# Performance work log

Hardware: AMD Instinct MI355X
Metric: run time of the kernel (lower is better)

Reference implementation:

```python
import jax, jax.numpy as jnp
import numpy as np

B, N, D = 4, 2048, 512
H, DH = 8, 64  # heads, dim_head; inner_dim = H*DH = 512
SCALE = DH ** -0.5


def setup_inputs() -> dict:
    key = jax.random.key(0)
    kx, kw = jax.random.split(key)
    x = jax.random.normal(kx, (B, N, D), dtype=jnp.float32)
    # torch Linear weight layout: [out_features=3*H*DH, in_features=D]
    W_qkv = jax.random.normal(kw, (3 * H * DH, D), dtype=jnp.float32) * 0.02
    return {"x": x, "W_qkv": W_qkv}


def reference(x, W_qkv):
    b, n, d = x.shape
    # qkv projection (no bias since qkv_bias=False)
    qkv = x @ W_qkv.T                                  # [b, n, 3*H*DH]
    qkv = qkv.reshape(b, n, 3, H, DH).transpose(2, 0, 3, 1, 4)  # [3, b, H, n, DH]
    q, k, v = qkv[0], qkv[1], qkv[2]
    # shifted query: q_cross[t] = q[t-1] for t>=1, q_cross[0] = q[0]
    q_cross = jnp.concatenate([q[:, :, :1, :], q[:, :, :-1, :]], axis=2)
    scores = jnp.einsum("bhqd,bhkd->bhqk", q_cross * SCALE, k)  # [b, H, n, n]
    attn = jax.nn.softmax(scores, axis=-1)
    out = jnp.einsum("bhqk,bhkd->bhqd", attn, v)       # [b, H, n, DH]
    out = out.transpose(0, 2, 1, 3).reshape(b, n, H * DH)
    # to_out is Dropout(0.0) -> identity in eval / p=0
    return out
```

## Files before the change

### kernel.cpp

```cpp
#include <hip/hip_runtime.h>
#include <hip/hip_bf16.h>
#include <stdint.h>

typedef __bf16 bf16_t;
typedef float floatx4 __attribute__((ext_vector_type(4)));
typedef __bf16 bf16x8 __attribute__((ext_vector_type(8)));
typedef __bf16 bf16x4 __attribute__((ext_vector_type(4)));
typedef unsigned int uintx4 __attribute__((ext_vector_type(4)));

#define QSCALE 0.1803368801111204f

__device__ __forceinline__ void gl2lds16(const bf16_t* g, bf16_t* l) {
    __builtin_amdgcn_global_load_lds(
        (const __attribute__((address_space(1))) unsigned int*)g,
        (__attribute__((address_space(3))) unsigned int*)l,
        16, 0, 0);
}

__device__ __forceinline__ unsigned pk2(float lo, float hi) {
    unsigned short a = __builtin_bit_cast(unsigned short, (bf16_t)lo);
    unsigned short b = __builtin_bit_cast(unsigned short, (bf16_t)hi);
    return (unsigned)a | ((unsigned)b << 16);
}

__global__ __launch_bounds__(256) void convert_kernel(const float* __restrict__ x,
                                                      bf16_t* __restrict__ xb,
                                                      const float* __restrict__ w,
                                                      bf16_t* __restrict__ wb,
                                                      int nx4) {
    int i = blockIdx.x * 256 + threadIdx.x;
    const float* in; bf16_t* out; int j;
    if (i < nx4) { in = x; out = xb; j = i; }
    else         { in = w; out = wb; j = i - nx4; }
    float4 v = ((const float4*)in)[j];
    bf16x4 o;
    o.x = (bf16_t)v.x; o.y = (bf16_t)v.y; o.z = (bf16_t)v.z; o.w = (bf16_t)v.w;
    ((bf16x4*)out)[j] = o;
}

__global__ __launch_bounds__(256, 3) void qkv_gemm(const bf16_t* __restrict__ X,
                                                   const bf16_t* __restrict__ W,
                                                   bf16_t* __restrict__ Q,
                                                   bf16_t* __restrict__ K,
                                                   bf16_t* __restrict__ Vt)
{
    __shared__ bf16_t As[2][128 * 64];
    __shared__ bf16_t Bs[2][64 * 64];

    const int tid  = threadIdx.x;
    const int wave = tid >> 6;
    const int lane = tid & 63;
    const int quad = lane >> 4;
    const int lrow = lane & 15;
    const int t7g  = lrow & 7;
    const int wbase = tid & 192;

    int raw = blockIdx.x;
    int xcd = raw & 7;
    int idx = raw >> 3;
    int bx  = xcd * 8 + idx / 24;
    int by  = idx - (idx / 24) * 24;
    const int bm0 = bx * 128;
    const int bn0 = by * 64;
    const int mw = (wave >> 1) * 64;
    const int nw = (wave & 1) * 32;

    floatx4 acc[4][2];
#pragma unroll
    for (int i = 0; i < 4; i++)
#pragma unroll
        for (int j = 0; j < 2; j++) acc[i][j] = (floatx4)0.0f;

    const bf16_t* xb  = X + (size_t)bm0 * 512;
    const bf16_t* wbp = W + (size_t)bn0 * 512;
    const bf16_t* srcA[4];
    const bf16_t* srcB[2];
#pragma unroll
    for (int r = 0; r < 4; ++r) {
        int c = r * 256 + tid;
        int row = c >> 3, kc = c & 7;
        int skc = kc ^ (row & 7);
        srcA[r] = xb + (size_t)row * 512 + skc * 8;
    }
#pragma unroll
    for (int r = 0; r < 2; ++r) {
        int c = r * 256 + tid;
        int row = c >> 3, kc = c & 7;
        int skc = kc ^ (row & 7);
        srcB[r] = wbp + (size_t)row * 512 + skc * 8;
    }

    auto STAGE = [&](int bufI, int k0) {
#pragma unroll
        for (int r = 0; r < 4; ++r)
            gl2lds16(srcA[r] + k0, As[bufI] + (size_t)(r * 256 + wbase) * 8);
#pragma unroll
        for (int r = 0; r < 2; ++r)
            gl2lds16(srcB[r] + k0, Bs[bufI] + (size_t)(r * 256 + wbase) * 8);
    };

    STAGE(0, 0);

#pragma unroll 1
    for (int kb = 0; kb < 8; ++kb) {
        const int buf = kb & 1;
        __syncthreads();
        if (kb < 7) STAGE(buf ^ 1, (kb + 1) * 64);

        const bf16_t* as = As[buf];
        const bf16_t* bs = Bs[buf];
#pragma unroll
        for (int ks = 0; ks < 2; ++ks) {
            bf16x8 af[4], bfr[2];
#pragma unroll
            for (int mi = 0; mi < 4; mi++)
                af[mi] = *(const bf16x8*)(as + (mw + mi * 16 + lrow) * 64 + (((ks * 4 + quad) ^ t7g) << 3));
#pragma unroll
            for (int ni = 0; ni < 2; ni++)
                bfr[ni] = *(const bf16x8*)(bs + (nw + ni * 16 + lrow) * 64 + (((ks * 4 + quad) ^ t7g) << 3));
            __builtin_amdgcn_s_setprio(1);
#pragma unroll
            for (int mi = 0; mi < 4; mi++)
#pragma unroll
                for (int ni = 0; ni < 2; ni++)
                    acc[mi][ni] = __builtin_amdgcn_mfma_f32_16x16x32_bf16(af[mi], bfr[ni], acc[mi][ni], 0, 0, 0);
            __builtin_amdgcn_s_setprio(0);
        }
    }

#pragma unroll
    for (int mi = 0; mi < 4; mi++) {
        int mbase = bm0 + mw + mi * 16 + quad * 4;
        int b = mbase >> 11, n = mbase & 2047;
#pragma unroll
        for (int ni = 0; ni < 2; ni++) {
            int o = bn0 + nw + ni * 16 + lrow;
            int s  = o >> 9;
            int h  = (o >> 6) & 7;
            int dh = o & 63;
            int bh = b * 8 + h;
            if (s == 2) {
                bf16x4 pv;
#pragma unroll
                for (int r = 0; r < 4; r++) pv[r] = (bf16_t)acc[mi][ni][r];
                *(bf16x4*)(Vt + ((size_t)bh * 64 + dh) * 2048 + n) = pv;
            } else if (s == 0) {
#pragma unroll
                for (int r = 0; r < 4; r++)
                    Q[((size_t)bh * 2048 + n + r) * 64 + dh] = (bf16_t)(acc[mi][ni][r] * QSCALE);
            } else {
#pragma unroll
                for (int r = 0; r < 4; r++)
                    K[((size_t)bh * 2048 + n + r) * 64 + dh] = (bf16_t)acc[mi][ni][r];
            }
        }
    }
}

__device__ __forceinline__ void stage_tile(const bf16_t* __restrict__ kb,
                                           const bf16_t* __restrict__ vb,
                                           int kt, bf16_t* ksbuf, bf16_t* vsbuf,
                                           int wave, int lane) {
#pragma unroll
    for (int part = 0; part < 2; ++part) {
        int ch  = part * 256 + wave * 64 + lane;
        int row = ch >> 3, cc = ch & 7;
        int scc = cc ^ (row & 7);
        bf16_t* ldst = ksbuf + (size_t)(part * 256 + wave * 64) * 8;
        gl2lds16(kb + ((size_t)(kt * 64 + row)) * 64 + scc * 8, ldst);
        bf16_t* ldst2 = vsbuf + (size_t)(part * 256 + wave * 64) * 8;
        gl2lds16(vb + (size_t)row * 2048 + kt * 64 + scc * 8, ldst2);
    }
}

__global__ __launch_bounds__(256, 5) void flash_attn(const bf16_t* __restrict__ Q,
                                                     const bf16_t* __restrict__ K,
                                                     const bf16_t* __restrict__ Vt,
                                                     float* __restrict__ Out)
{
    __shared__ bf16_t Ks[2][64 * 64];
    __shared__ bf16_t Vs[2][64 * 64];

    const int tid  = threadIdx.x;
    const int wave = tid >> 6;
    const int lane = tid & 63;
    const int quad = lane >> 4;
    const int c    = lane & 15;
    const int t7   = c & 7;
    const int qhalf = wave >> 1;
    const int khalf = wave & 1;

    int raw = blockIdx.x + (blockIdx.y << 5);
    int swz = (raw & 7) * 128 + (raw >> 3);
    const int qt = swz & 31;
    const int bh = swz >> 5;
    const int b = bh >> 3, h = bh & 7;

    const int bw    = ((c & 4) << 1) | ((c & 8) >> 1) | (c & 3);
    const int brow7 = bw & 7;

    bf16x8 qf[2][2];
#pragma unroll
    for (int mt = 0; mt < 2; ++mt) {
        int qg  = qt * 64 + qhalf * 32 + mt * 16 + c;
        int src = (qg == 0) ? 0 : qg - 1;
        const bf16_t* qbase = Q + ((size_t)bh * 2048 + src) * 64;
        qf[mt][0] = *(const bf16x8*)(qbase + quad * 8);
        qf[mt][1] = *(const bf16x8*)(qbase + 32 + quad * 8);
    }

    floatx4 o[2][4];
#pragma unroll
    for (int mt = 0; mt < 2; ++mt)
#pragma unroll
        for (int i = 0; i < 4; i++) o[mt][i] = (floatx4)0.0f;
    float lacc[2] = {0.f, 0.f};

    const bf16_t* kb = K + ((size_t)bh * 2048) * 64;
    const bf16_t* vb = Vt + ((size_t)bh * 64) * 2048;

    stage_tile(kb, vb, 0, Ks[0], Vs[0], wave, lane);

#pragma unroll 1
    for (int kt = 0; kt < 32; ++kt) {
        const int buf = kt & 1;
        __syncthreads();
        if (kt < 31)
            stage_tile(kb, vb, kt + 1, Ks[buf ^ 1], Vs[buf ^ 1], wave, lane);

        const bf16_t* ks = Ks[buf];
        const bf16_t* vs = Vs[buf];

        floatx4 s[2][2];
        __builtin_amdgcn_s_setprio(1);
#pragma unroll
        for (int nt = 0; nt < 2; ++nt) {
            const bf16_t* krow = ks + (khalf * 32 + nt * 16 + bw) * 64;
            bf16x8 kf0 = *(const bf16x8*)(krow + ((quad ^ brow7) << 3));
            bf16x8 kf1 = *(const bf16x8*)(krow + (((4 + quad) ^ brow7) << 3));
#pragma unroll
            for (int mt = 0; mt < 2; ++mt) {
                floatx4 t = (floatx4)0.0f;
                t = __builtin_amdgcn_mfma_f32_16x16x32_bf16(kf0, qf[mt][0], t, 0, 0, 0);
                t = __builtin_amdgcn_mfma_f32_16x16x32_bf16(kf1, qf[mt][1], t, 0, 0, 0);
                s[mt][nt] = t;
            }
        }
        __builtin_amdgcn_s_setprio(0);

        bf16x8 pfrag[2];
#pragma unroll
        for (int mt = 0; mt < 2; ++mt) {
            float pe[2][4];
#pragma unroll
            for (int nt = 0; nt < 2; ++nt)
#pragma unroll
                for (int r = 0; r < 4; ++r) {
                    float p = __builtin_amdgcn_exp2f(s[mt][nt][r]);
                    lacc[mt] += p;
                    pe[nt][r] = p;
                }
            unsigned A0 = pk2(pe[0][0], pe[0][1]);
            unsigned A1 = pk2(pe[0][2], pe[0][3]);
            unsigned B0 = pk2(pe[1][0], pe[1][1]);
            unsigned B1 = pk2(pe[1][2], pe[1][3]);
            auto r0 = __builtin_amdgcn_permlane32_swap((int)A0, (int)B0, false, false);
            auto r1 = __builtin_amdgcn_permlane32_swap((int)A1, (int)B1, false, false);
            uintx4 fd;
            fd.x = (unsigned)r0[0];
            fd.y = (unsigned)r1[0];
            fd.z = (unsigned)r0[1];
            fd.w = (unsigned)r1[1];
            pfrag[mt] = __builtin_bit_cast(bf16x8, fd);
        }

        __builtin_amdgcn_s_setprio(1);
#pragma unroll
        for (int sub = 0; sub < 4; ++sub) {
            const bf16_t* vrow = vs + (sub * 16 + c) * 64;
            bf16x8 vf = *(const bf16x8*)(vrow + (((khalf * 4 + quad) ^ t7) << 3));
            o[0][sub] = __builtin_amdgcn_mfma_f32_16x16x32_bf16(pfrag[0], vf, o[0][sub], 0, 0, 0);
            o[1][sub] = __builtin_amdgcn_mfma_f32_16x16x32_bf16(pfrag[1], vf, o[1][sub], 0, 0, 0);
        }
        __builtin_amdgcn_s_setprio(0);
    }

#pragma unroll
    for (int mt = 0; mt < 2; ++mt) {
        lacc[mt] += __shfl_xor(lacc[mt], 16, 64);
        lacc[mt] += __shfl_xor(lacc[mt], 32, 64);
    }

    __syncthreads();
    float* obuf = (float*)Ks;
    float* lbuf = (float*)Vs;
    if (khalf == 1) {
#pragma unroll
        for (int mt = 0; mt < 2; ++mt)
#pragma unroll
            for (int sub = 0; sub < 4; ++sub)
                *(floatx4*)(obuf + qhalf * 2048 + (mt * 4 + sub) * 256 + lane * 4) = o[mt][sub];
        if (lane < 16) {
#pragma unroll
            for (int mt = 0; mt < 2; ++mt)
                lbuf[qhalf * 32 + mt * 16 + c] = lacc[mt];
        }
    }
    __syncthreads();
    if (khalf == 0) {
#pragma unroll
        for (int mt = 0; mt < 2; ++mt)
#pragma unroll
            for (int sub = 0; sub < 4; ++sub)
                o[mt][sub] += *(const floatx4*)(obuf + qhalf * 2048 + (mt * 4 + sub) * 256 + lane * 4);
#pragma unroll
        for (int mt = 0; mt < 2; ++mt)
            lacc[mt] += lbuf[qhalf * 32 + mt * 16 + c];

        float* ob = Out + (size_t)b * 2048 * 512 + (size_t)h * 64;
#pragma unroll
        for (int mt = 0; mt < 2; ++mt) {
            int n0 = qt * 64 + qhalf * 32 + mt * 16 + quad * 4;
#pragma unroll
            for (int r = 0; r < 4; r++) {
                float lr = __shfl(lacc[mt], quad * 4 + r, 64);
                float inv = 1.0f / lr;
                float* orow = ob + (size_t)(n0 + r) * 512;
#pragma unroll
                for (int sub = 0; sub < 4; ++sub)
                    orow[sub * 16 + c] = o[mt][sub][r] * inv;
            }
        }
    }
}

extern "C" void kernel_launch(void* const* d_in, const int* in_sizes, int n_in,
                              void* d_out, int out_size, void* d_ws, size_t ws_size,
                              hipStream_t stream) {
    const float* x = (const float*)d_in[0];
    const float* w = (const float*)d_in[1];
    float* out = (float*)d_out;

    char* ws = (char*)d_ws;
    bf16_t* xb = (bf16_t*)(ws);
    bf16_t* wb = (bf16_t*)(ws + 8388608);
    bf16_t* q  = (bf16_t*)(ws + 9961472);
    bf16_t* k  = (bf16_t*)(ws + 18350080);
    bf16_t* vt = (bf16_t*)(ws + 26738688);

    convert_kernel<<<4864, 256, 0, stream>>>(x, xb, w, wb, 1048576);
    qkv_gemm<<<1536, 256, 0, stream>>>(xb, wb, q, k, vt);
    flash_attn<<<dim3(32, 32), 256, 0, stream>>>(q, k, vt, out);
}
```

Measured before the change: 140.9 us.

## Load K and V fragments directly from global memory, dropping LDS staging

Removes the double-buffered LDS staging of K and V tiles and the per-iteration block barrier. Each wave now loads its MFMA fragments straight from global memory into registers and relies on L2/L1 for reuse across the waves that share a head. The occupancy hint drops from 5 to 4 blocks. This saves LDS traffic and synchronisation, but global load latency is now exposed inside the loop with no software prefetch, and each K/V row is fetched by multiple waves.

```diff
diff --git a/kernel.cpp b/kernel.cpp
--- a/kernel.cpp
+++ b/kernel.cpp
@@ -157,36 +157,18 @@
     }
 }
 
-__device__ __forceinline__ void stage_tile(const bf16_t* __restrict__ kb,
-                                           const bf16_t* __restrict__ vb,
-                                           int kt, bf16_t* ksbuf, bf16_t* vsbuf,
-                                           int wave, int lane) {
-#pragma unroll
-    for (int part = 0; part < 2; ++part) {
-        int ch  = part * 256 + wave * 64 + lane;
-        int row = ch >> 3, cc = ch & 7;
-        int scc = cc ^ (row & 7);
-        bf16_t* ldst = ksbuf + (size_t)(part * 256 + wave * 64) * 8;
-        gl2lds16(kb + ((size_t)(kt * 64 + row)) * 64 + scc * 8, ldst);
-        bf16_t* ldst2 = vsbuf + (size_t)(part * 256 + wave * 64) * 8;
-        gl2lds16(vb + (size_t)row * 2048 + kt * 64 + scc * 8, ldst2);
-    }
-}
-
-__global__ __launch_bounds__(256, 5) void flash_attn(const bf16_t* __restrict__ Q,
+__global__ __launch_bounds__(256, 4) void flash_attn(const bf16_t* __restrict__ Q,
                                                      const bf16_t* __restrict__ K,
                                                      const bf16_t* __restrict__ Vt,
                                                      float* __restrict__ Out)
 {
-    __shared__ bf16_t Ks[2][64 * 64];
-    __shared__ bf16_t Vs[2][64 * 64];
+    __shared__ float red[2 * 2048 + 64];
 
     const int tid  = threadIdx.x;
     const int wave = tid >> 6;
     const int lane = tid & 63;
     const int quad = lane >> 4;
     const int c    = lane & 15;
-    const int t7   = c & 7;
     const int qhalf = wave >> 1;
     const int khalf = wave & 1;
 
@@ -196,8 +178,7 @@
     const int bh = swz >> 5;
     const int b = bh >> 3, h = bh & 7;
 
-    const int bw    = ((c & 4) << 1) | ((c & 8) >> 1) | (c & 3);
-    const int brow7 = bw & 7;
+    const int bw = ((c & 4) << 1) | ((c & 8) >> 1) | (c & 3);
 
     bf16x8 qf[2][2];
 #pragma unroll
@@ -216,37 +197,36 @@
         for (int i = 0; i < 4; i++) o[mt][i] = (floatx4)0.0f;
     float lacc[2] = {0.f, 0.f};
 
-    const bf16_t* kb = K + ((size_t)bh * 2048) * 64;
-    const bf16_t* vb = Vt + ((size_t)bh * 64) * 2048;
-
-    stage_tile(kb, vb, 0, Ks[0], Vs[0], wave, lane);
+    const bf16_t* kk = K + ((size_t)bh * 2048 + khalf * 32 + bw) * 64 + quad * 8;
+    const bf16_t* vv = Vt + ((size_t)bh * 64 + c) * 2048 + khalf * 32 + quad * 8;
 
 #pragma unroll 1
     for (int kt = 0; kt < 32; ++kt) {
-        const int buf = kt & 1;
-        __syncthreads();
-        if (kt < 31)
-            stage_tile(kb, vb, kt + 1, Ks[buf ^ 1], Vs[buf ^ 1], wave, lane);
-
-        const bf16_t* ks = Ks[buf];
-        const bf16_t* vs = Vs[buf];
+        bf16x8 kf00 = *(const bf16x8*)(kk);
+        bf16x8 kf01 = *(const bf16x8*)(kk + 32);
+        bf16x8 kf10 = *(const bf16x8*)(kk + 1024);
+        bf16x8 kf11 = *(const bf16x8*)(kk + 1056);
 
         floatx4 s[2][2];
         __builtin_amdgcn_s_setprio(1);
 #pragma unroll
-        for (int nt = 0; nt < 2; ++nt) {
-            const bf16_t* krow = ks + (khalf * 32 + nt * 16 + bw) * 64;
-            bf16x8 kf0 = *(const bf16x8*)(krow + ((quad ^ brow7) << 3));
-            bf16x8 kf1 = *(const bf16x8*)(krow + (((4 + quad) ^ brow7) << 3));
-#pragma unroll
-            for (int mt = 0; mt < 2; ++mt) {
-                floatx4 t = (floatx4)0.0f;
-                t = __builtin_amdgcn_mfma_f32_16x16x32_bf16(kf0, qf[mt][0], t, 0, 0, 0);
-                t = __builtin_amdgcn_mfma_f32_16x16x32_bf16(kf1, qf[mt][1], t, 0, 0, 0);
-                s[mt][nt] = t;
-            }
+        for (int mt = 0; mt < 2; ++mt) {
+            floatx4 t0 = (floatx4)0.0f;
+            t0 = __builtin_amdgcn_mfma_f32_16x16x32_bf16(kf00, qf[mt][0], t0, 0, 0, 0);
+            t0 = __builtin_amdgcn_mfma_f32_16x16x32_bf16(kf01, qf[mt][1], t0, 0, 0, 0);
+            s[mt][0] = t0;
+            floatx4 t1 = (floatx4)0.0f;
+            t1 = __builtin_amdgcn_mfma_f32_16x16x32_bf16(kf10, qf[mt][0], t1, 0, 0, 0);
+            t1 = __builtin_amdgcn_mfma_f32_16x16x32_bf16(kf11, qf[mt][1], t1, 0, 0, 0);
+            s[mt][1] = t1;
         }
         __builtin_amdgcn_s_setprio(0);
+
+        bf16x8 vf0 = *(const bf16x8*)(vv);
+        bf16x8 vf1 = *(const bf16x8*)(vv + 16 * 2048);
+        bf16x8 vf2 = *(const bf16x8*)(vv + 32 * 2048);
+        bf16x8 vf3 = *(const bf16x8*)(vv + 48 * 2048);
+        kk += 4096; vv += 64;
 
         bf16x8 pfrag[2];
 #pragma unroll
@@ -275,13 +255,14 @@
         }
 
         __builtin_amdgcn_s_setprio(1);
-#pragma unroll
-        for (int sub = 0; sub < 4; ++sub) {
-            const bf16_t* vrow = vs + (sub * 16 + c) * 64;
-            bf16x8 vf = *(const bf16x8*)(vrow + (((khalf * 4 + quad) ^ t7) << 3));
-            o[0][sub] = __builtin_amdgcn_mfma_f32_16x16x32_bf16(pfrag[0], vf, o[0][sub], 0, 0, 0);
-            o[1][sub] = __builtin_amdgcn_mfma_f32_16x16x32_bf16(pfrag[1], vf, o[1][sub], 0, 0, 0);
-        }
+        o[0][0] = __builtin_amdgcn_mfma_f32_16x16x32_bf16(pfrag[0], vf0, o[0][0], 0, 0, 0);
+        o[1][0] = __builtin_amdgcn_mfma_f32_16x16x32_bf16(pfrag[1], vf0, o[1][0], 0, 0, 0);
+        o[0][1] = __builtin_amdgcn_mfma_f32_16x16x32_bf16(pfrag[0], vf1, o[0][1], 0, 0, 0);
+        o[1][1] = __builtin_amdgcn_mfma_f32_16x16x32_bf16(pfrag[1], vf1, o[1][1], 0, 0, 0);
+        o[0][2] = __builtin_amdgcn_mfma_f32_16x16x32_bf16(pfrag[0], vf2, o[0][2], 0, 0, 0);
+        o[1][2] = __builtin_amdgcn_mfma_f32_16x16x32_bf16(pfrag[1], vf2, o[1][2], 0, 0, 0);
+        o[0][3] = __builtin_amdgcn_mfma_f32_16x16x32_bf16(pfrag[0], vf3, o[0][3], 0, 0, 0);
+        o[1][3] = __builtin_amdgcn_mfma_f32_16x16x32_bf16(pfrag[1], vf3, o[1][3], 0, 0, 0);
         __builtin_amdgcn_s_setprio(0);
     }
 
@@ -291,9 +272,8 @@
         lacc[mt] += __shfl_xor(lacc[mt], 32, 64);
     }
 
-    __syncthreads();
-    float* obuf = (float*)Ks;
-    float* lbuf = (float*)Vs;
+    float* obuf = red;
+    float* lbuf = red + 4096;
     if (khalf == 1) {
 #pragma unroll
         for (int mt = 0; mt < 2; ++mt)
```

Result: slower. 209.0 us (+48.4%).

## Split keys across all four waves with 128-key stages and tree reduction

Applied to the files above, without the earlier changes.

Each wave now handles all 64 queries of the block against its own 16-key slice of each 64-key tile, instead of a 2x2 split over queries and keys. Two K/V tiles (128 keys) are loaded per iteration without double buffering, with a barrier before and after each load. A two-level LDS reduction then merges the four partial outputs. This halves the loop trip count and increases reuse of each loaded K/V fragment. In exchange the load latency is exposed, register pressure rises (launch bounds drop from 5 to 3), the epilogue reduction is longer, and the block-index swizzle is removed.

```diff
diff --git a/kernel.cpp b/kernel.cpp
--- a/kernel.cpp
+++ b/kernel.cpp
@@ -157,113 +157,112 @@
     }
 }
 
-__device__ __forceinline__ void stage_tile(const bf16_t* __restrict__ kb,
-                                           const bf16_t* __restrict__ vb,
-                                           int kt, bf16_t* ksbuf, bf16_t* vsbuf,
-                                           int wave, int lane) {
-#pragma unroll
-    for (int part = 0; part < 2; ++part) {
-        int ch  = part * 256 + wave * 64 + lane;
-        int row = ch >> 3, cc = ch & 7;
-        int scc = cc ^ (row & 7);
-        bf16_t* ldst = ksbuf + (size_t)(part * 256 + wave * 64) * 8;
-        gl2lds16(kb + ((size_t)(kt * 64 + row)) * 64 + scc * 8, ldst);
-        bf16_t* ldst2 = vsbuf + (size_t)(part * 256 + wave * 64) * 8;
-        gl2lds16(vb + (size_t)row * 2048 + kt * 64 + scc * 8, ldst2);
-    }
-}
-
-__global__ __launch_bounds__(256, 5) void flash_attn(const bf16_t* __restrict__ Q,
+__global__ __launch_bounds__(256, 3) void flash_attn(const bf16_t* __restrict__ Q,
                                                      const bf16_t* __restrict__ K,
                                                      const bf16_t* __restrict__ Vt,
                                                      float* __restrict__ Out)
 {
-    __shared__ bf16_t Ks[2][64 * 64];
-    __shared__ bf16_t Vs[2][64 * 64];
+    __shared__ __align__(16) bf16_t smem[4 * 4096];
+    __shared__ float lbuf[4 * 64];
+
+    bf16_t* Ks = smem;
+    bf16_t* Vs = smem + 8192;
 
     const int tid  = threadIdx.x;
-    const int wave = tid >> 6;
+    const int w    = tid >> 6;
     const int lane = tid & 63;
     const int quad = lane >> 4;
     const int c    = lane & 15;
-    const int t7   = c & 7;
-    const int qhalf = wave >> 1;
-    const int khalf = wave & 1;
-
-    int raw = blockIdx.x + (blockIdx.y << 5);
-    int swz = (raw & 7) * 128 + (raw >> 3);
-    const int qt = swz & 31;
-    const int bh = swz >> 5;
-    const int b = bh >> 3, h = bh & 7;
-
-    const int bw    = ((c & 4) << 1) | ((c & 8) >> 1) | (c & 3);
-    const int brow7 = bw & 7;
-
-    bf16x8 qf[2][2];
-#pragma unroll
-    for (int mt = 0; mt < 2; ++mt) {
-        int qg  = qt * 64 + qhalf * 32 + mt * 16 + c;
+    const int qt = blockIdx.x;
+    const int bh = blockIdx.y;
+    const int b = bh >> 3, hd = bh & 7;
+
+    const int bw  = ((c & 4) << 1) | ((c & 8) >> 1) | (c & 3);
+    const int bw7 = bw & 7;
+
+    bf16x8 qf[4][2];
+#pragma unroll
+    for (int g = 0; g < 4; ++g) {
+        int qg  = qt * 64 + g * 16 + c;
         int src = (qg == 0) ? 0 : qg - 1;
         const bf16_t* qbase = Q + ((size_t)bh * 2048 + src) * 64;
-        qf[mt][0] = *(const bf16x8*)(qbase + quad * 8);
-        qf[mt][1] = *(const bf16x8*)(qbase + 32 + quad * 8);
-    }
-
-    floatx4 o[2][4];
-#pragma unroll
-    for (int mt = 0; mt < 2; ++mt)
-#pragma unroll
-        for (int i = 0; i < 4; i++) o[mt][i] = (floatx4)0.0f;
-    float lacc[2] = {0.f, 0.f};
+#pragma unroll
+        for (int h = 0; h < 2; ++h)
+            qf[g][h] = *(const bf16x8*)(qbase + h * 32 + quad * 8);
+    }
+
+    floatx4 O[4][4];
+#pragma unroll
+    for (int g = 0; g < 4; ++g)
+#pragma unroll
+        for (int dg = 0; dg < 4; ++dg) O[g][dg] = (floatx4)0.0f;
+    float lacc[4] = {0.f, 0.f, 0.f, 0.f};
 
     const bf16_t* kb = K + ((size_t)bh * 2048) * 64;
     const bf16_t* vb = Vt + ((size_t)bh * 64) * 2048;
 
-    stage_tile(kb, vb, 0, Ks[0], Vs[0], wave, lane);
+    const int ch0 = w * 64 + lane;
+    const int r0s = ch0 >> 3, c0s = (ch0 & 7) ^ (r0s & 7);
+    const int ch1 = 256 + ch0;
+    const int r1s = ch1 >> 3, c1s = (ch1 & 7) ^ (r1s & 7);
+    const bf16_t* gk0 = kb + r0s * 64 + c0s * 8;
+    const bf16_t* gk1 = kb + r1s * 64 + c1s * 8;
+    const bf16_t* gv0 = vb + (size_t)r0s * 2048 + c0s * 8;
+    const bf16_t* gv1 = vb + (size_t)r1s * 2048 + c1s * 8;
+    const int woff = w * 512;
+
+    const int krow = w * 16 + bw;
+    int koff[2][2];
+#pragma unroll
+    for (int t = 0; t < 2; ++t)
+#pragma unroll
+        for (int h = 0; h < 2; ++h)
+            koff[t][h] = t * 4096 + krow * 64 + (((h * 4 + quad) ^ bw7) << 3);
+    int voff[4];
+#pragma unroll
+    for (int dg = 0; dg < 4; ++dg)
+        voff[dg] = (quad >> 1) * 4096 + (dg * 16 + c) * 64 + (((2 * w + (quad & 1)) ^ (c & 7)) << 3);
 
 #pragma unroll 1
-    for (int kt = 0; kt < 32; ++kt) {
-        const int buf = kt & 1;
+    for (int p = 0; p < 16; ++p) {
         __syncthreads();
-        if (kt < 31)
-            stage_tile(kb, vb, kt + 1, Ks[buf ^ 1], Vs[buf ^ 1], wave, lane);
-
-        const bf16_t* ks = Ks[buf];
-        const bf16_t* vs = Vs[buf];
-
-        floatx4 s[2][2];
-        __builtin_amdgcn_s_setprio(1);
-#pragma unroll
-        for (int nt = 0; nt < 2; ++nt) {
-            const bf16_t* krow = ks + (khalf * 32 + nt * 16 + bw) * 64;
-            bf16x8 kf0 = *(const bf16x8*)(krow + ((quad ^ brow7) << 3));
-            bf16x8 kf1 = *(const bf16x8*)(krow + (((4 + quad) ^ brow7) << 3));
-#pragma unroll
-            for (int mt = 0; mt < 2; ++mt) {
-                floatx4 t = (floatx4)0.0f;
-                t = __builtin_amdgcn_mfma_f32_16x16x32_bf16(kf0, qf[mt][0], t, 0, 0, 0);
-                t = __builtin_amdgcn_mfma_f32_16x16x32_bf16(kf1, qf[mt][1], t, 0, 0, 0);
-                s[mt][nt] = t;
+#pragma unroll
+        for (int t = 0; t < 2; ++t) {
+            const int kt = 2 * p + t;
+            gl2lds16(gk0 + (size_t)kt * 4096, Ks + t * 4096 + woff);
+            gl2lds16(gk1 + (size_t)kt * 4096, Ks + t * 4096 + 2048 + woff);
+            gl2lds16(gv0 + kt * 64,           Vs + t * 4096 + woff);
+            gl2lds16(gv1 + kt * 64,           Vs + t * 4096 + 2048 + woff);
+        }
+        __syncthreads();
+
+        bf16x8 kf00 = *(const bf16x8*)(Ks + koff[0][0]);
+        bf16x8 kf01 = *(const bf16x8*)(Ks + koff[0][1]);
+        bf16x8 kf10 = *(const bf16x8*)(Ks + koff[1][0]);
+        bf16x8 kf11 = *(const bf16x8*)(Ks + koff[1][1]);
+
+        bf16x8 pfrag[4];
+#pragma unroll
+        for (int g = 0; g < 4; ++g) {
+            __builtin_amdgcn_s_setprio(1);
+            floatx4 s0 = (floatx4)0.0f, s1 = (floatx4)0.0f;
+            s0 = __builtin_amdgcn_mfma_f32_16x16x32_bf16(kf00, qf[g][0], s0, 0, 0, 0);
+            s0 = __builtin_amdgcn_mfma_f32_16x16x32_bf16(kf01, qf[g][1], s0, 0, 0, 0);
+            s1 = __builtin_amdgcn_mfma_f32_16x16x32_bf16(kf10, qf[g][0], s1, 0, 0, 0);
+            s1 = __builtin_amdgcn_mfma_f32_16x16x32_bf16(kf11, qf[g][1], s1, 0, 0, 0);
+            __builtin_amdgcn_s_setprio(0);
+
+            float p0[4], p1[4];
+#pragma unroll
+            for (int r = 0; r < 4; ++r) {
+                p0[r] = __builtin_amdgcn_exp2f(s0[r]);
+                p1[r] = __builtin_amdgcn_exp2f(s1[r]);
+                lacc[g] += p0[r] + p1[r];
             }
-        }
-        __builtin_amdgcn_s_setprio(0);
-
-        bf16x8 pfrag[2];
-#pragma unroll
-        for (int mt = 0; mt < 2; ++mt) {
-            float pe[2][4];
-#pragma unroll
-            for (int nt = 0; nt < 2; ++nt)
-#pragma unroll
-                for (int r = 0; r < 4; ++r) {
-                    float p = __builtin_amdgcn_exp2f(s[mt][nt][r]);
-                    lacc[mt] += p;
-                    pe[nt][r] = p;
-                }
-            unsigned A0 = pk2(pe[0][0], pe[0][1]);
-            unsigned A1 = pk2(pe[0][2], pe[0][3]);
-            unsigned B0 = pk2(pe[1][0], pe[1][1]);
-            unsigned B1 = pk2(pe[1][2], pe[1][3]);
+            unsigned A0 = pk2(p0[0], p0[1]);
+            unsigned A1 = pk2(p0[2], p0[3]);
+            unsigned B0 = pk2(p1[0], p1[1]);
+            unsigned B1 = pk2(p1[2], p1[3]);
             auto r0 = __builtin_amdgcn_permlane32_swap((int)A0, (int)B0, false, false);
             auto r1 = __builtin_amdgcn_permlane32_swap((int)A1, (int)B1, false, false);
             uintx4 fd;
@@ -271,64 +270,81 @@
             fd.y = (unsigned)r1[0];
             fd.z = (unsigned)r0[1];
             fd.w = (unsigned)r1[1];
-            pfrag[mt] = __builtin_bit_cast(bf16x8, fd);
+            pfrag[g] = __builtin_bit_cast(bf16x8, fd);
         }
 
         __builtin_amdgcn_s_setprio(1);
 #pragma unroll
-        for (int sub = 0; sub < 4; ++sub) {
-            const bf16_t* vrow = vs + (sub * 16 + c) * 64;
-            bf16x8 vf = *(const bf16x8*)(vrow + (((khalf * 4 + quad) ^ t7) << 3));
-            o[0][sub] = __builtin_amdgcn_mfma_f32_16x16x32_bf16(pfrag[0], vf, o[0][sub], 0, 0, 0);
-            o[1][sub] = __builtin_amdgcn_mfma_f32_16x16x32_bf16(pfrag[1], vf, o[1][sub], 0, 0, 0);
+        for (int dg = 0; dg < 4; ++dg) {
+            bf16x8 vf = *(const bf16x8*)(Vs + voff[dg]);
+#pragma unroll
+            for (int g = 0; g < 4; ++g)
+                O[g][dg] = __builtin_amdgcn_mfma_f32_16x16x32_bf16(pfrag[g], vf, O[g][dg], 0, 0, 0);
         }
         __builtin_amdgcn_s_setprio(0);
     }
 
 #pragma unroll
-    for (int mt = 0; mt < 2; ++mt) {
-        lacc[mt] += __shfl_xor(lacc[mt], 16, 64);
-        lacc[mt] += __shfl_xor(lacc[mt], 32, 64);
-    }
-
+    for (int g = 0; g < 4; ++g) {
+        lacc[g] += __shfl_xor(lacc[g], 16, 64);
+        lacc[g] += __shfl_xor(lacc[g], 32, 64);
+    }
+    if (lane < 16) {
+#pragma unroll
+        for (int g = 0; g < 4; ++g)
+            lbuf[w * 64 + g * 16 + lane] = lacc[g];
+    }
+
+    float* obuf = (float*)smem;
     __syncthreads();
-    float* obuf = (float*)Ks;
-    float* lbuf = (float*)Vs;
-    if (khalf == 1) {
-#pragma unroll
-        for (int mt = 0; mt < 2; ++mt)
-#pragma unroll
-            for (int sub = 0; sub < 4; ++sub)
-                *(floatx4*)(obuf + qhalf * 2048 + (mt * 4 + sub) * 256 + lane * 4) = o[mt][sub];
-        if (lane < 16) {
-#pragma unroll
-            for (int mt = 0; mt < 2; ++mt)
-                lbuf[qhalf * 32 + mt * 16 + c] = lacc[mt];
-        }
+    if (w & 1) {
+        float* dst = obuf + (w >> 1) * 4096;
+#pragma unroll
+        for (int g = 0; g < 4; ++g)
+#pragma unroll
+            for (int dg = 0; dg < 4; ++dg)
+                *(floatx4*)(dst + (g * 4 + dg) * 256 + lane * 4) = O[g][dg];
     }
     __syncthreads();
-    if (khalf == 0) {
-#pragma unroll
-        for (int mt = 0; mt < 2; ++mt)
-#pragma unroll
-            for (int sub = 0; sub < 4; ++sub)
-                o[mt][sub] += *(const floatx4*)(obuf + qhalf * 2048 + (mt * 4 + sub) * 256 + lane * 4);
-#pragma unroll
-        for (int mt = 0; mt < 2; ++mt)
-            lacc[mt] += lbuf[qhalf * 32 + mt * 16 + c];
-
-        float* ob = Out + (size_t)b * 2048 * 512 + (size_t)h * 64;
-#pragma unroll
-        for (int mt = 0; mt < 2; ++mt) {
-            int n0 = qt * 64 + qhalf * 32 + mt * 16 + quad * 4;
-#pragma unroll
-            for (int r = 0; r < 4; r++) {
-                float lr = __shfl(lacc[mt], quad * 4 + r, 64);
+    if (!(w & 1)) {
+        const float* src = obuf + (w >> 1) * 4096;
+#pragma unroll
+        for (int g = 0; g < 4; ++g)
+#pragma unroll
+            for (int dg = 0; dg < 4; ++dg)
+                O[g][dg] += *(const floatx4*)(src + (g * 4 + dg) * 256 + lane * 4);
+    }
+    __syncthreads();
+    if (w == 2) {
+        float* dst = obuf + 4096;
+#pragma unroll
+        for (int g = 0; g < 4; ++g)
+#pragma unroll
+            for (int dg = 0; dg < 4; ++dg)
+                *(floatx4*)(dst + (g * 4 + dg) * 256 + lane * 4) = O[g][dg];
+    }
+    __syncthreads();
+    if (w == 0) {
+        const float* src = obuf + 4096;
+#pragma unroll
+        for (int g = 0; g < 4; ++g)
+#pragma unroll
+            for (int dg = 0; dg < 4; ++dg)
+                O[g][dg] += *(const floatx4*)(src + (g * 4 + dg) * 256 + lane * 4);
+
+        float* ob = Out + (size_t)b * 2048 * 512 + (size_t)hd * 64;
+#pragma unroll
+        for (int g = 0; g < 4; ++g) {
+            float lt = lbuf[0 * 64 + g * 16 + c] + lbuf[1 * 64 + g * 16 + c]
+                     + lbuf[2 * 64 + g * 16 + c] + lbuf[3 * 64 + g * 16 + c];
+#pragma unroll
+            for (int r = 0; r < 4; ++r) {
+                float lr = __shfl(lt, quad * 4 + r, 64);
                 float inv = 1.0f / lr;
-                float* orow = ob + (size_t)(n0 + r) * 512;
-#pragma unroll
-                for (int sub = 0; sub < 4; ++sub)
-                    orow[sub * 16 + c] = o[mt][sub][r] * inv;
+                float* orow = ob + (size_t)(qt * 64 + g * 16 + quad * 4 + r) * 512;
+#pragma unroll
+                for (int dg = 0; dg < 4; ++dg)
+                    orow[dg * 16 + c] = O[g][dg][r] * inv;
             }
         }
     }
```

Result: slower. 143.8 us (+2.1%).
